# Kernel tuning notes

Hardware: AMD Instinct MI355X
Metric: run time of the kernel (lower is better)

Reference implementation:

```python
import jax, jax.numpy as jnp
import numpy as np

B, T, D = 64, 512, 1024

def setup_inputs() -> dict:
    key = jax.random.key(0)
    k1, k2, k3 = jax.random.split(key, 3)
    q1 = jax.random.normal(k1, (B, T, D), dtype=jnp.float32)
    q2 = jax.random.normal(k2, (B, T, D), dtype=jnp.float32)
    # original uses 'uniform' init; scale like a small uniform weight
    U = jax.random.uniform(k3, (D, D), dtype=jnp.float32, minval=-0.05, maxval=0.05)
    return {"q1": q1, "q2": q2, "U": U}

def reference(q1, q2, U):
    # bilinear scores: (q1 @ U) @ q2^T -> [B, T1, T2]
    att = jnp.einsum('btd,de,bse->bts', q1, U, q2)
    att = jax.nn.relu(att)
    w1_att = jax.nn.softmax(att, axis=1)  # softmax over q1 timesteps
    w2_att = jax.nn.softmax(att, axis=2)  # softmax over q2 timesteps
    # q1_align = w1_att^T @ q1 -> [B, T2, D]
    q1_align = jnp.einsum('bts,btd->bsd', w1_att, q1)
    # q2_align = w2_att @ q2 -> [B, T1, D]
    q2_align = jnp.einsum('bts,bsd->btd', w2_att, q2)
    return (q1_align, q2_align)
```

## Files before the change

kernel.cpp:

```cpp
#include <hip/hip_runtime.h>
#include <hip/hip_bf16.h>
#include <math.h>

#define B_DIM 64
#define T_DIM 512
#define D_DIM 1024
#define TT (T_DIM * T_DIM)
#define TD (T_DIM * D_DIM)
#define PSTR ((long)B_DIM * T_DIM)

typedef _Float16 f16;
typedef f16 f16x4 __attribute__((ext_vector_type(4)));
typedef f16 f16x8 __attribute__((ext_vector_type(8)));
typedef float f32x4 __attribute__((ext_vector_type(4)));

__device__ __forceinline__ void gld_lds16(const void* g, void* l) {
    __builtin_amdgcn_global_load_lds(
        (const __attribute__((address_space(1))) void*)g,
        (__attribute__((address_space(3))) void*)l, 16, 0, 0);
}

#define SWZ(r) (((r) >> 1) & 3)

__global__ __launch_bounds__(256) void k_d1(const float* __restrict__ q1,
                                            f16* __restrict__ q1ht,
                                            const float* __restrict__ U,
                                            f16* __restrict__ Uht) {
    __shared__ f16 tr[64][72];
    int tid = threadIdx.x;
    int z = blockIdx.z;
    if (z < 64) {
        int b = z;
        int d0 = blockIdx.x * 64, t0 = blockIdx.y * 64;
        const float* S = q1 + ((size_t)b * T_DIM + t0) * D_DIM + d0;
        int rr = tid >> 4, cc = (tid & 15) * 4;
#pragma unroll
        for (int i = 0; i < 4; ++i) {
            int r = rr + i * 16;
            float4 v = *(const float4*)(S + (size_t)r * D_DIM + cc);
            tr[cc + 0][r] = (f16)v.x;
            tr[cc + 1][r] = (f16)v.y;
            tr[cc + 2][r] = (f16)v.z;
            tr[cc + 3][r] = (f16)v.w;
        }
        __syncthreads();
        f16* Dt = q1ht + ((size_t)b * D_DIM + d0) * T_DIM + t0;
        int r2 = tid >> 3, c8 = (tid & 7) * 8;
#pragma unroll
        for (int i = 0; i < 2; ++i) {
            int d = r2 + i * 32;
            f16x8 vv = *(const f16x8*)(&tr[d][c8]);
            *(f16x8*)(Dt + (size_t)d * T_DIM + c8) = vv;
        }
    } else {
        int pos = blockIdx.y * 16 + blockIdx.x;
        for (int u = 0; u < 2; ++u) {
            int tile = pos + u * 128;
            int n0 = (tile & 15) * 64, k0 = (tile >> 4) * 64;
            int rr = tid >> 4, cc = (tid & 15) * 4;
#pragma unroll
            for (int i = 0; i < 4; ++i) {
                int r = rr + i * 16;
                float4 v = *(const float4*)(U + (size_t)(k0 + r) * D_DIM + n0 + cc);
                tr[cc + 0][r] = (f16)v.x;
                tr[cc + 1][r] = (f16)v.y;
                tr[cc + 2][r] = (f16)v.z;
                tr[cc + 3][r] = (f16)v.w;
            }
            __syncthreads();
            int r2 = tid >> 3, c8 = (tid & 7) * 8;
#pragma unroll
            for (int i = 0; i < 2; ++i) {
                int n = r2 + i * 32;
                f16x8 vv = *(const f16x8*)(&tr[n][c8]);
                *(f16x8*)(Uht + (size_t)(n0 + n) * D_DIM + k0 + c8) = vv;
            }
            __syncthreads();
        }
    }
}

__global__ __launch_bounds__(512, 2) void k_d2(const float* __restrict__ q1,
                                               const f16* __restrict__ Uht,
                                               f16* __restrict__ qUh,
                                               const float* __restrict__ q2,
                                               f16* __restrict__ q2h,
                                               f16* __restrict__ q2ht) {
    __shared__ __align__(16) f16 SM[32768];
    int tid = threadIdx.x;
    if (blockIdx.y < 128) {
        f16 (*LA)[8192] = (f16(*)[8192])SM;
        f16 (*LB)[8192] = (f16(*)[8192])(SM + 16384);
        const int lane = tid & 63, w = tid >> 6;
        int o = blockIdx.x + 4 * blockIdx.y;
        int fl = (o & 7) * 64 + (o >> 3);
        int bx = fl & 3, by = fl >> 2;
        const float* Aq = q1 + (long)(by * 256) * D_DIM;
        const f16* Bb = Uht + (long)(bx * 256) * D_DIM;

        const int r0 = tid >> 2, j0 = tid & 3;
        const int r1 = r0 + 128;
        const long srcA0 = (long)r0 * D_DIM + j0 * 8;
        const long srcA1 = (long)r1 * D_DIM + j0 * 8;
        const int wA0 = r0 * 32 + ((j0 ^ SWZ(r0)) << 3);
        const int wA1 = r1 * 32 + ((j0 ^ SWZ(r1)) << 3);
        const long offB0 = (long)r0 * D_DIM + (j0 ^ SWZ(r0)) * 8;
        const long offB1 = (long)r1 * D_DIM + (j0 ^ SWZ(r1)) * 8;
        const int ldsOff0 = w * 512, ldsOff1 = 4096 + w * 512;
        const int g = lane >> 4;
        const int rA0 = (w & 1) * 128 + (lane & 15);
        const int rB0 = (w >> 1) * 64 + (lane & 15);

        f32x4 acc[8][4] = {};
        {
            float4 v0 = *(const float4*)(Aq + srcA0);
            float4 v1 = *(const float4*)(Aq + srcA0 + 4);
            float4 v2 = *(const float4*)(Aq + srcA1);
            float4 v3 = *(const float4*)(Aq + srcA1 + 4);
            f16x8 h0 = {(f16)v0.x, (f16)v0.y, (f16)v0.z, (f16)v0.w,
                        (f16)v1.x, (f16)v1.y, (f16)v1.z, (f16)v1.w};
            f16x8 h1 = {(f16)v2.x, (f16)v2.y, (f16)v2.z, (f16)v2.w,
                        (f16)v3.x, (f16)v3.y, (f16)v3.z, (f16)v3.w};
            *(f16x8*)(&LA[0][wA0]) = h0;
            *(f16x8*)(&LA[0][wA1]) = h1;
            gld_lds16(Bb + offB0, &LB[0][ldsOff0]);
            gld_lds16(Bb + offB1, &LB[0][ldsOff1]);
        }
        __syncthreads();

        for (int t = 0; t < 32; ++t) {
            const int cur = t & 1;
            float4 v0, v1, v2, v3;
            if (t + 1 < 32) {
                const long kc = (long)(t + 1) << 5;
                v0 = *(const float4*)(Aq + srcA0 + kc);
                v1 = *(const float4*)(Aq + srcA0 + kc + 4);
                v2 = *(const float4*)(Aq + srcA1 + kc);
                v3 = *(const float4*)(Aq + srcA1 + kc + 4);
                gld_lds16(Bb + offB0 + kc, &LB[cur ^ 1][ldsOff0]);
                gld_lds16(Bb + offB1 + kc, &LB[cur ^ 1][ldsOff1]);
            }
            f16x8 a[8], b[4];
#pragma unroll
            for (int m = 0; m < 8; ++m) {
                int r = rA0 + m * 16;
                a[m] = *(const f16x8*)(&LA[cur][r * 32 + ((g ^ SWZ(r)) << 3)]);
            }
#pragma unroll
            for (int n = 0; n < 4; ++n) {
                int r = rB0 + n * 16;
                b[n] = *(const f16x8*)(&LB[cur][r * 32 + ((g ^ SWZ(r)) << 3)]);
            }
            __builtin_amdgcn_s_setprio(1);
#pragma unroll
            for (int m = 0; m < 8; ++m)
#pragma unroll
                for (int n = 0; n < 4; ++n)
                    acc[m][n] = __builtin_amdgcn_mfma_f32_16x16x32_f16(a[m], b[n], acc[m][n], 0, 0, 0);
            __builtin_amdgcn_s_setprio(0);
            if (t + 1 < 32) {
                f16x8 h0 = {(f16)v0.x, (f16)v0.y, (f16)v0.z, (f16)v0.w,
                            (f16)v1.x, (f16)v1.y, (f16)v1.z, (f16)v1.w};
                f16x8 h1 = {(f16)v2.x, (f16)v2.y, (f16)v2.z, (f16)v2.w,
                            (f16)v3.x, (f16)v3.y, (f16)v3.z, (f16)v3.w};
                *(f16x8*)(&LA[cur ^ 1][wA0]) = h0;
                *(f16x8*)(&LA[cur ^ 1][wA1]) = h1;
            }
            __syncthreads();
        }
        const int row0 = by * 256 + (w & 1) * 128 + (lane >> 4) * 4;
        const int col0 = bx * 256 + (w >> 1) * 64 + (lane & 15);
#pragma unroll
        for (int m = 0; m < 8; ++m)
#pragma unroll
            for (int r = 0; r < 4; ++r) {
                long row = row0 + m * 16 + r;
#pragma unroll
                for (int n = 0; n < 4; ++n)
                    qUh[row * D_DIM + col0 + n * 16] = (f16)acc[m][n][r];
            }
    } else {
        int hf = tid >> 8, t2 = tid & 255;
        f16 (*tr)[72] = (f16(*)[72])(SM + hf * 4608);
        int p = (blockIdx.y - 128) * 4 + blockIdx.x;
        int tile = p * 2 + hf;
        int b = tile >> 7, rem = tile & 127;
        int d0 = (rem & 15) * 64, t0 = (rem >> 4) * 64;
        const float* S = q2 + ((size_t)b * T_DIM + t0) * D_DIM + d0;
        f16* Dr = q2h + ((size_t)b * T_DIM + t0) * D_DIM + d0;
        int rr = t2 >> 4, cc = (t2 & 15) * 4;
#pragma unroll
        for (int i = 0; i < 4; ++i) {
            int r = rr + i * 16;
            float4 v = *(const float4*)(S + (size_t)r * D_DIM + cc);
            f16x4 h = {(f16)v.x, (f16)v.y, (f16)v.z, (f16)v.w};
            *(f16x4*)(Dr + (size_t)r * D_DIM + cc) = h;
            tr[cc + 0][r] = h[0];
            tr[cc + 1][r] = h[1];
            tr[cc + 2][r] = h[2];
            tr[cc + 3][r] = h[3];
        }
        __syncthreads();
        f16* Dt = q2ht + ((size_t)b * D_DIM + d0) * T_DIM + t0;
        int r2 = t2 >> 3, c8 = (t2 & 7) * 8;
#pragma unroll
        for (int i = 0; i < 2; ++i) {
            int d = r2 + i * 32;
            f16x8 vv = *(const f16x8*)(&tr[d][c8]);
            *(f16x8*)(Dt + (size_t)d * T_DIM + c8) = vv;
        }
    }
}

__global__ __launch_bounds__(512, 2) void k_att3(const f16* __restrict__ qUh,
                                                 const f16* __restrict__ q2h,
                                                 f16* __restrict__ P2,
                                                 f16* __restrict__ P1,
                                                 float2* __restrict__ rowP,
                                                 float2* __restrict__ colP) {
    __shared__ __align__(16) f16 LA[2][8192];
    __shared__ __align__(16) f16 LB[2][8192];
    const int tid = threadIdx.x;
    const int lane = tid & 63, w = tid >> 6;

    int o = blockIdx.x + 2 * (blockIdx.y + 2 * blockIdx.z);
    int fl = (o & 7) * 32 + (o >> 3);
    const int bx = fl & 1, by = (fl >> 1) & 1, zb = fl >> 2;

    const f16* Ab = qUh + (long)(zb * 512 + by * 256) * D_DIM;
    const f16* Bb = q2h + (long)zb * TD + (long)(bx * 256) * D_DIM;

    const int r0 = tid >> 2, j0 = tid & 3;
    const int r1 = r0 + 128;
    const long offA0 = (long)r0 * D_DIM + (j0 ^ SWZ(r0)) * 8;
    const long offA1 = (long)r1 * D_DIM + (j0 ^ SWZ(r1)) * 8;
    const int ldsOff0 = w * 512, ldsOff1 = 4096 + w * 512;
    const int g = lane >> 4;
    const int rA0 = (w & 1) * 128 + (lane & 15);
    const int rB0 = (w >> 1) * 64 + (lane & 15);

    f32x4 acc[8][4] = {};

    gld_lds16(Ab + offA0, &LA[0][ldsOff0]);
    gld_lds16(Ab + offA1, &LA[0][ldsOff1]);
    gld_lds16(Bb + offA0, &LB[0][ldsOff0]);
    gld_lds16(Bb + offA1, &LB[0][ldsOff1]);
    __syncthreads();

    for (int t = 0; t < 32; ++t) {
        const int cur = t & 1;
        if (t + 1 < 32) {
            const long kt = (long)(t + 1) << 5;
            gld_lds16(Ab + offA0 + kt, &LA[cur ^ 1][ldsOff0]);
            gld_lds16(Ab + offA1 + kt, &LA[cur ^ 1][ldsOff1]);
            gld_lds16(Bb + offA0 + kt, &LB[cur ^ 1][ldsOff0]);
            gld_lds16(Bb + offA1 + kt, &LB[cur ^ 1][ldsOff1]);
        }
        f16x8 a[8], b[4];
#pragma unroll
        for (int m = 0; m < 8; ++m) {
            int r = rA0 + m * 16;
            a[m] = *(const f16x8*)(&LA[cur][r * 32 + ((g ^ SWZ(r)) << 3)]);
        }
#pragma unroll
        for (int n = 0; n < 4; ++n) {
            int r = rB0 + n * 16;
            b[n] = *(const f16x8*)(&LB[cur][r * 32 + ((g ^ SWZ(r)) << 3)]);
        }
        __builtin_amdgcn_s_setprio(1);
#pragma unroll
        for (int m = 0; m < 8; ++m)
#pragma unroll
            for (int n = 0; n < 4; ++n)
                acc[m][n] = __builtin_amdgcn_mfma_f32_16x16x32_f16(a[m], b[n], acc[m][n], 0, 0, 0);
        __builtin_amdgcn_s_setprio(0);
        __syncthreads();
    }

#pragma unroll
    for (int m = 0; m < 8; ++m)
#pragma unroll
        for (int n = 0; n < 4; ++n)
#pragma unroll
            for (int r = 0; r < 4; ++r)
                acc[m][n][r] = fmaxf(acc[m][n][r], 0.0f);

    float* redR = (float*)(&LA[0][0]);
    float* redC = redR + 2048;
    float* rowM = redC + 1024;
    float* colM = rowM + 256;
    const int h = w & 1, cw = w >> 1;
#pragma unroll
    for (int m = 0; m < 8; ++m)
#pragma unroll
        for (int r = 0; r < 4; ++r) {
            float mx = fmaxf(fmaxf(acc[m][0][r], acc[m][1][r]),
                             fmaxf(acc[m][2][r], acc[m][3][r]));
            mx = fmaxf(mx, __shfl_xor(mx, 1));
            mx = fmaxf(mx, __shfl_xor(mx, 2));
            mx = fmaxf(mx, __shfl_xor(mx, 4));
            mx = fmaxf(mx, __shfl_xor(mx, 8));
            float sm = __expf(acc[m][0][r] - mx) + __expf(acc[m][1][r] - mx)
                     + __expf(acc[m][2][r] - mx) + __expf(acc[m][3][r] - mx);
            sm += __shfl_xor(sm, 1);
            sm += __shfl_xor(sm, 2);
            sm += __shfl_xor(sm, 4);
            sm += __shfl_xor(sm, 8);
            if ((lane & 15) == 0) {
                int lr = m * 16 + (lane >> 4) * 4 + r;
                redR[((h * 128 + lr) * 4 + cw) * 2 + 0] = mx;
                redR[((h * 128 + lr) * 4 + cw) * 2 + 1] = sm;
            }
        }
#pragma unroll
    for (int n = 0; n < 4; ++n) {
        float mx = acc[0][n][0];
#pragma unroll
        for (int m = 0; m < 8; ++m)
#pragma unroll
            for (int r = 0; r < 4; ++r) mx = fmaxf(mx, acc[m][n][r]);
        mx = fmaxf(mx, __shfl_xor(mx, 16));
        mx = fmaxf(mx, __shfl_xor(mx, 32));
        float sm = 0.f;
#pragma unroll
        for (int m = 0; m < 8; ++m)
#pragma unroll
            for (int r = 0; r < 4; ++r) sm += __expf(acc[m][n][r] - mx);
        sm += __shfl_xor(sm, 16);
        sm += __shfl_xor(sm, 32);
        if (lane < 16) {
            int c = cw * 64 + n * 16 + lane;
            redC[(h * 256 + c) * 2 + 0] = mx;
            redC[(h * 256 + c) * 2 + 1] = sm;
        }
    }
    __syncthreads();
    if (tid < 256) {
        float M = -1e30f, S = 0.f;
#pragma unroll
        for (int i = 0; i < 4; ++i) {
            float m_ = redR[(tid * 4 + i) * 2 + 0];
            float s_ = redR[(tid * 4 + i) * 2 + 1];
            float nm = fmaxf(M, m_);
            S = S * __expf(M - nm) + s_ * __expf(m_ - nm);
            M = nm;
        }
        rowP[(long)bx * PSTR + (long)zb * 512 + by * 256 + tid] = make_float2(M, S);
        rowM[tid] = M;
    } else {
        int c = tid - 256;
        float m0_ = redC[c * 2 + 0], s0_ = redC[c * 2 + 1];
        float m1_ = redC[(256 + c) * 2 + 0], s1_ = redC[(256 + c) * 2 + 1];
        float M = fmaxf(m0_, m1_);
        float S = s0_ * __expf(m0_ - M) + s1_ * __expf(m1_ - M);
        colP[(long)by * PSTR + (long)zb * 512 + bx * 256 + c] = make_float2(M, S);
        colM[c] = M;
    }
    __syncthreads();

    f16* P2b = P2 + (long)zb * TT;
#pragma unroll
    for (int m = 0; m < 8; ++m)
#pragma unroll
        for (int r = 0; r < 4; ++r) {
            int Lr = h * 128 + m * 16 + (lane >> 4) * 4 + r;
            float M = rowM[Lr];
            long base = (long)(by * 256 + Lr) * T_DIM + bx * 256;
#pragma unroll
            for (int n = 0; n < 4; ++n) {
                int c = cw * 64 + n * 16 + (lane & 15);
                P2b[base + c] = (f16)__expf(acc[m][n][r] - M);
            }
        }
    f16* P1b = P1 + (long)zb * TT;
#pragma unroll
    for (int m = 0; m < 8; ++m) {
        int Lt = h * 128 + m * 16 + (lane >> 4) * 4;
#pragma unroll
        for (int n = 0; n < 4; ++n) {
            int Lc = cw * 64 + n * 16 + (lane & 15);
            float M = colM[Lc];
            f16x4 v = {(f16)__expf(acc[m][n][0] - M), (f16)__expf(acc[m][n][1] - M),
                       (f16)__expf(acc[m][n][2] - M), (f16)__expf(acc[m][n][3] - M)};
            *(f16x4*)(&P1b[(long)(bx * 256 + Lc) * T_DIM + by * 256 + Lt]) = v;
        }
    }
}

__global__ __launch_bounds__(512, 2) void k_align(
        const f16* __restrict__ P2, const f16* __restrict__ q2ht,
        const float2* __restrict__ rowP, float* __restrict__ outQ2,
        const f16* __restrict__ P1, const f16* __restrict__ q1ht,
        const float2* __restrict__ colP, float* __restrict__ outQ1) {
    __shared__ __align__(16) f16 LA[2][8192];
    __shared__ __align__(16) f16 LB[2][8192];
    const int tid = threadIdx.x;
    const int lane = tid & 63, w = tid >> 6;

    int o = blockIdx.x + 4 * (blockIdx.y + 2 * blockIdx.z);
    int fl = (o & 7) * 128 + (o >> 3);
    const int bx = fl & 3, by = (fl >> 2) & 1, z = fl >> 3;
    const int zb = z & 63;

    const f16* P  = (z < 64) ? P2 : P1;
    const f16* Bt = (z < 64) ? q2ht : q1ht;
    const float2* sp = ((z < 64) ? rowP : colP) + (long)zb * 512;
    float* out = ((z < 64) ? outQ2 : outQ1) + (long)zb * TD;

    const f16* Ab = P + (long)zb * TT + (long)(by * 256) * T_DIM;
    const f16* Bb = Bt + (long)zb * TD + (long)(bx * 256) * T_DIM;

    const int r0 = tid >> 2, j0 = tid & 3;
    const int r1 = r0 + 128;
    float2 pa0 = sp[by * 256 + r0], pb0 = sp[PSTR + by * 256 + r0];
    float M0 = fmaxf(pa0.x, pb0.x);
    f16 f00 = (f16)__expf(pa0.x - M0), f01 = (f16)__expf(pb0.x - M0);
    float2 pa1 = sp[by * 256 + r1], pb1 = sp[PSTR + by * 256 + r1];
    float M1 = fmaxf(pa1.x, pb1.x);
    f16 f10 = (f16)__expf(pa1.x - M1), f11 = (f16)__expf(pb1.x - M1);

    const long srcA0 = (long)r0 * T_DIM + j0 * 8;
    const long srcA1 = (long)r1 * T_DIM + j0 * 8;
    const int wA0 = r0 * 32 + ((j0 ^ SWZ(r0)) << 3);
    const int wA1 = r1 * 32 + ((j0 ^ SWZ(r1)) << 3);
    const long offB0 = (long)r0 * T_DIM + (j0 ^ SWZ(r0)) * 8;
    const long offB1 = (long)r1 * T_DIM + (j0 ^ SWZ(r1)) * 8;
    const int ldsOff0 = w * 512, ldsOff1 = 4096 + w * 512;
    const int g = lane >> 4;
    const int rA0 = (w & 1) * 128 + (lane & 15);
    const int rB0 = (w >> 1) * 64 + (lane & 15);

    f32x4 acc[8][4] = {};
    {
        f16x8 a0 = *(const f16x8*)(Ab + srcA0);
        f16x8 a1 = *(const f16x8*)(Ab + srcA1);
#pragma unroll
        for (int i = 0; i < 8; ++i) { a0[i] *= f00; a1[i] *= f10; }
        *(f16x8*)(&LA[0][wA0]) = a0;
        *(f16x8*)(&LA[0][wA1]) = a1;
        gld_lds16(Bb + offB0, &LB[0][ldsOff0]);
        gld_lds16(Bb + offB1, &LB[0][ldsOff1]);
    }
    __syncthreads();

    for (int t = 0; t < 16; ++t) {
        const int cur = t & 1;
        f16x8 a0n, a1n;
        if (t + 1 < 16) {
            const long kc = (long)(t + 1) << 5;
            a0n = *(const f16x8*)(Ab + srcA0 + kc);
            a1n = *(const f16x8*)(Ab + srcA1 + kc);
            gld_lds16(Bb + offB0 + kc, &LB[cur ^ 1][ldsOff0]);
            gld_lds16(Bb + offB1 + kc, &LB[cur ^ 1][ldsOff1]);
        }
        f16x8 a[8], b[4];
#pragma unroll
        for (int m = 0; m < 8; ++m) {
            int r = rA0 + m * 16;
            a[m] = *(const f16x8*)(&LA[cur][r * 32 + ((g ^ SWZ(r)) << 3)]);
        }
#pragma unroll
        for (int n = 0; n < 4; ++n) {
            int r = rB0 + n * 16;
            b[n] = *(const f16x8*)(&LB[cur][r * 32 + ((g ^ SWZ(r)) << 3)]);
        }
        __builtin_amdgcn_s_setprio(1);
#pragma unroll
        for (int m = 0; m < 8; ++m)
#pragma unroll
            for (int n = 0; n < 4; ++n)
                acc[m][n] = __builtin_amdgcn_mfma_f32_16x16x32_f16(a[m], b[n], acc[m][n], 0, 0, 0);
        __builtin_amdgcn_s_setprio(0);
        if (t + 1 < 16) {
            f16 fa = ((t + 1) & 8) ? f01 : f00;
            f16 fb = ((t + 1) & 8) ? f11 : f10;
#pragma unroll
            for (int i = 0; i < 8; ++i) { a0n[i] *= fa; a1n[i] *= fb; }
            *(f16x8*)(&LA[cur ^ 1][wA0]) = a0n;
            *(f16x8*)(&LA[cur ^ 1][wA1]) = a1n;
        }
        __syncthreads();
    }

    const int row0 = by * 256 + (w & 1) * 128 + (lane >> 4) * 4;
    const int col0 = bx * 256 + (w >> 1) * 64 + (lane & 15);
#pragma unroll
    for (int m = 0; m < 8; ++m)
#pragma unroll
        for (int r = 0; r < 4; ++r) {
            int row = row0 + m * 16 + r;
            float2 pa = sp[row], pb = sp[PSTR + row];
            float M = fmaxf(pa.x, pb.x);
            float S = pa.y * __expf(pa.x - M) + pb.y * __expf(pb.x - M);
            float inv = 1.0f / S;
#pragma unroll
            for (int n = 0; n < 4; ++n)
                out[(long)row * D_DIM + col0 + n * 16] = acc[m][n][r] * inv;
        }
}

extern "C" void kernel_launch(void* const* d_in, const int* in_sizes, int n_in,
                              void* d_out, int out_size, void* d_ws, size_t ws_size,
                              hipStream_t stream) {
    const float* q1 = (const float*)d_in[0];
    const float* q2 = (const float*)d_in[1];
    const float* U  = (const float*)d_in[2];
    float* out = (float*)d_out;

    const size_t BTD = (size_t)B_DIM * TD;
    const size_t DD  = (size_t)D_DIM * D_DIM;
    const size_t BTT = (size_t)B_DIM * TT;

    const size_t need = (4 * BTD + DD) * 2
                      + 2 * BTT * 2
                      + 4 * (size_t)PSTR * sizeof(float2);
    if (need > ws_size) return;

    f16* q1ht = (f16*)d_ws;
    f16* q2h  = q1ht + BTD;
    f16* q2ht = q2h  + BTD;
    f16* Uht  = q2ht + BTD;
    f16* qUh  = Uht  + DD;
    f16* P2   = qUh  + BTD;
    f16* P1   = P2   + BTT;
    float2* rowP = (float2*)(P1 + BTT);
    float2* colP = rowP + 2 * (size_t)PSTR;

    k_d1<<<dim3(16, 8, 65), 256, 0, stream>>>(q1, q1ht, U, Uht);
    k_d2<<<dim3(4, 128 + 1024, 1), 512, 0, stream>>>(q1, Uht, qUh, q2, q2h, q2ht);
    k_att3<<<dim3(2, 2, 64), 512, 0, stream>>>(qUh, q2h, P2, P1, rowP, colP);
    k_align<<<dim3(4, 2, 128), 512, 0, stream>>>(
        P2, q2ht, rowP, out + BTD, P1, q1ht, colP, out);
}
```

Measured before the change: 387.6 us.

## Drop q2 fp16 copy; cast q2 inside attention GEMM and move transpose into cast kernel

The row-major fp16 copy of q2 (q2h) is no longer materialized. The attention-score kernel now reads q2 as fp32 from global memory and converts it to fp16 in registers before the swizzled LDS store, the same way the first GEMM already handles q1. The q2 transpose-cast moves into the first cast kernel alongside q1, so the qU GEMM kernel no longer shares a launch with the cast blocks. This removes a BTD-sized fp16 write and read, but k_att3 now reads fp32 (twice the bytes) for its B operand and does register conversions instead of direct global-to-LDS loads.

```diff
diff --git a/kernel.cpp b/kernel.cpp
--- a/kernel.cpp
+++ b/kernel.cpp
@@ -22,17 +22,21 @@
 
 #define SWZ(r) (((r) >> 1) & 3)
 
-__global__ __launch_bounds__(256) void k_d1(const float* __restrict__ q1,
-                                            f16* __restrict__ q1ht,
-                                            const float* __restrict__ U,
-                                            f16* __restrict__ Uht) {
+__global__ __launch_bounds__(256) void k_cast(const float* __restrict__ q1,
+                                              f16* __restrict__ q1ht,
+                                              const float* __restrict__ q2,
+                                              f16* __restrict__ q2ht,
+                                              const float* __restrict__ U,
+                                              f16* __restrict__ Uht) {
     __shared__ f16 tr[64][72];
     int tid = threadIdx.x;
     int z = blockIdx.z;
-    if (z < 64) {
-        int b = z;
+    if (z < 128) {
+        const float* src = (z < 64) ? q1 : q2;
+        f16* dstT = (z < 64) ? q1ht : q2ht;
+        int b = z & 63;
         int d0 = blockIdx.x * 64, t0 = blockIdx.y * 64;
-        const float* S = q1 + ((size_t)b * T_DIM + t0) * D_DIM + d0;
+        const float* S = src + ((size_t)b * T_DIM + t0) * D_DIM + d0;
         int rr = tid >> 4, cc = (tid & 15) * 4;
 #pragma unroll
         for (int i = 0; i < 4; ++i) {
@@ -44,7 +48,7 @@
             tr[cc + 3][r] = (f16)v.w;
         }
         __syncthreads();
-        f16* Dt = q1ht + ((size_t)b * D_DIM + d0) * T_DIM + t0;
+        f16* Dt = dstT + ((size_t)b * D_DIM + d0) * T_DIM + t0;
         int r2 = tid >> 3, c8 = (tid & 7) * 8;
 #pragma unroll
         for (int i = 0; i < 2; ++i) {
@@ -80,140 +84,104 @@
     }
 }
 
-__global__ __launch_bounds__(512, 2) void k_d2(const float* __restrict__ q1,
-                                               const f16* __restrict__ Uht,
-                                               f16* __restrict__ qUh,
-                                               const float* __restrict__ q2,
-                                               f16* __restrict__ q2h,
-                                               f16* __restrict__ q2ht) {
-    __shared__ __align__(16) f16 SM[32768];
-    int tid = threadIdx.x;
-    if (blockIdx.y < 128) {
-        f16 (*LA)[8192] = (f16(*)[8192])SM;
-        f16 (*LB)[8192] = (f16(*)[8192])(SM + 16384);
-        const int lane = tid & 63, w = tid >> 6;
-        int o = blockIdx.x + 4 * blockIdx.y;
-        int fl = (o & 7) * 64 + (o >> 3);
-        int bx = fl & 3, by = fl >> 2;
-        const float* Aq = q1 + (long)(by * 256) * D_DIM;
-        const f16* Bb = Uht + (long)(bx * 256) * D_DIM;
-
-        const int r0 = tid >> 2, j0 = tid & 3;
-        const int r1 = r0 + 128;
-        const long srcA0 = (long)r0 * D_DIM + j0 * 8;
-        const long srcA1 = (long)r1 * D_DIM + j0 * 8;
-        const int wA0 = r0 * 32 + ((j0 ^ SWZ(r0)) << 3);
-        const int wA1 = r1 * 32 + ((j0 ^ SWZ(r1)) << 3);
-        const long offB0 = (long)r0 * D_DIM + (j0 ^ SWZ(r0)) * 8;
-        const long offB1 = (long)r1 * D_DIM + (j0 ^ SWZ(r1)) * 8;
-        const int ldsOff0 = w * 512, ldsOff1 = 4096 + w * 512;
-        const int g = lane >> 4;
-        const int rA0 = (w & 1) * 128 + (lane & 15);
-        const int rB0 = (w >> 1) * 64 + (lane & 15);
-
-        f32x4 acc[8][4] = {};
-        {
-            float4 v0 = *(const float4*)(Aq + srcA0);
-            float4 v1 = *(const float4*)(Aq + srcA0 + 4);
-            float4 v2 = *(const float4*)(Aq + srcA1);
-            float4 v3 = *(const float4*)(Aq + srcA1 + 4);
+__global__ __launch_bounds__(512, 2) void k_gemm1(const float* __restrict__ q1,
+                                                  const f16* __restrict__ Uht,
+                                                  f16* __restrict__ qUh) {
+    __shared__ __align__(16) f16 LA[2][8192];
+    __shared__ __align__(16) f16 LB[2][8192];
+    const int tid = threadIdx.x;
+    const int lane = tid & 63, w = tid >> 6;
+    int o = blockIdx.x + 4 * blockIdx.y;
+    int fl = (o & 7) * 64 + (o >> 3);
+    int bx = fl & 3, by = fl >> 2;
+    const float* Aq = q1 + (long)(by * 256) * D_DIM;
+    const f16* Bb = Uht + (long)(bx * 256) * D_DIM;
+
+    const int r0 = tid >> 2, j0 = tid & 3;
+    const int r1 = r0 + 128;
+    const long srcA0 = (long)r0 * D_DIM + j0 * 8;
+    const long srcA1 = (long)r1 * D_DIM + j0 * 8;
+    const int wA0 = r0 * 32 + ((j0 ^ SWZ(r0)) << 3);
+    const int wA1 = r1 * 32 + ((j0 ^ SWZ(r1)) << 3);
+    const long offB0 = (long)r0 * D_DIM + (j0 ^ SWZ(r0)) * 8;
+    const long offB1 = (long)r1 * D_DIM + (j0 ^ SWZ(r1)) * 8;
+    const int ldsOff0 = w * 512, ldsOff1 = 4096 + w * 512;
+    const int g = lane >> 4;
+    const int rA0 = (w & 1) * 128 + (lane & 15);
+    const int rB0 = (w >> 1) * 64 + (lane & 15);
+
+    f32x4 acc[8][4] = {};
+    {
+        float4 v0 = *(const float4*)(Aq + srcA0);
+        float4 v1 = *(const float4*)(Aq + srcA0 + 4);
+        float4 v2 = *(const float4*)(Aq + srcA1);
+        float4 v3 = *(const float4*)(Aq + srcA1 + 4);
+        f16x8 h0 = {(f16)v0.x, (f16)v0.y, (f16)v0.z, (f16)v0.w,
+                    (f16)v1.x, (f16)v1.y, (f16)v1.z, (f16)v1.w};
+        f16x8 h1 = {(f16)v2.x, (f16)v2.y, (f16)v2.z, (f16)v2.w,
+                    (f16)v3.x, (f16)v3.y, (f16)v3.z, (f16)v3.w};
+        *(f16x8*)(&LA[0][wA0]) = h0;
+        *(f16x8*)(&LA[0][wA1]) = h1;
+        gld_lds16(Bb + offB0, &LB[0][ldsOff0]);
+        gld_lds16(Bb + offB1, &LB[0][ldsOff1]);
+    }
+    __syncthreads();
+
+    for (int t = 0; t < 32; ++t) {
+        const int cur = t & 1;
+        float4 v0, v1, v2, v3;
+        if (t + 1 < 32) {
+            const long kc = (long)(t + 1) << 5;
+            v0 = *(const float4*)(Aq + srcA0 + kc);
+            v1 = *(const float4*)(Aq + srcA0 + kc + 4);
+            v2 = *(const float4*)(Aq + srcA1 + kc);
+            v3 = *(const float4*)(Aq + srcA1 + kc + 4);
+            gld_lds16(Bb + offB0 + kc, &LB[cur ^ 1][ldsOff0]);
+            gld_lds16(Bb + offB1 + kc, &LB[cur ^ 1][ldsOff1]);
+        }
+        f16x8 a[8], b[4];
+#pragma unroll
+        for (int m = 0; m < 8; ++m) {
+            int r = rA0 + m * 16;
+            a[m] = *(const f16x8*)(&LA[cur][r * 32 + ((g ^ SWZ(r)) << 3)]);
+        }
+#pragma unroll
+        for (int n = 0; n < 4; ++n) {
+            int r = rB0 + n * 16;
+            b[n] = *(const f16x8*)(&LB[cur][r * 32 + ((g ^ SWZ(r)) << 3)]);
+        }
+        __builtin_amdgcn_s_setprio(1);
+#pragma unroll
+        for (int m = 0; m < 8; ++m)
+#pragma unroll
+            for (int n = 0; n < 4; ++n)
+                acc[m][n] = __builtin_amdgcn_mfma_f32_16x16x32_f16(a[m], b[n], acc[m][n], 0, 0, 0);
+        __builtin_amdgcn_s_setprio(0);
+        if (t + 1 < 32) {
             f16x8 h0 = {(f16)v0.x, (f16)v0.y, (f16)v0.z, (f16)v0.w,
                         (f16)v1.x, (f16)v1.y, (f16)v1.z, (f16)v1.w};
             f16x8 h1 = {(f16)v2.x, (f16)v2.y, (f16)v2.z, (f16)v2.w,
                         (f16)v3.x, (f16)v3.y, (f16)v3.z, (f16)v3.w};
-            *(f16x8*)(&LA[0][wA0]) = h0;
-            *(f16x8*)(&LA[0][wA1]) = h1;
-            gld_lds16(Bb + offB0, &LB[0][ldsOff0]);
-            gld_lds16(Bb + offB1, &LB[0][ldsOff1]);
+            *(f16x8*)(&LA[cur ^ 1][wA0]) = h0;
+            *(f16x8*)(&LA[cur ^ 1][wA1]) = h1;
         }
         __syncthreads();
-
-        for (int t = 0; t < 32; ++t) {
-            const int cur = t & 1;
-            float4 v0, v1, v2, v3;
-            if (t + 1 < 32) {
-                const long kc = (long)(t + 1) << 5;
-                v0 = *(const float4*)(Aq + srcA0 + kc);
-                v1 = *(const float4*)(Aq + srcA0 + kc + 4);
-                v2 = *(const float4*)(Aq + srcA1 + kc);
-                v3 = *(const float4*)(Aq + srcA1 + kc + 4);
-                gld_lds16(Bb + offB0 + kc, &LB[cur ^ 1][ldsOff0]);
-                gld_lds16(Bb + offB1 + kc, &LB[cur ^ 1][ldsOff1]);
-            }
-            f16x8 a[8], b[4];
-#pragma unroll
-            for (int m = 0; m < 8; ++m) {
-                int r = rA0 + m * 16;
-                a[m] = *(const f16x8*)(&LA[cur][r * 32 + ((g ^ SWZ(r)) << 3)]);
-            }
-#pragma unroll
-            for (int n = 0; n < 4; ++n) {
-                int r = rB0 + n * 16;
-                b[n] = *(const f16x8*)(&LB[cur][r * 32 + ((g ^ SWZ(r)) << 3)]);
-            }
-            __builtin_amdgcn_s_setprio(1);
-#pragma unroll
-            for (int m = 0; m < 8; ++m)
-#pragma unroll
-                for (int n = 0; n < 4; ++n)
-                    acc[m][n] = __builtin_amdgcn_mfma_f32_16x16x32_f16(a[m], b[n], acc[m][n], 0, 0, 0);
-            __builtin_amdgcn_s_setprio(0);
-            if (t + 1 < 32) {
-                f16x8 h0 = {(f16)v0.x, (f16)v0.y, (f16)v0.z, (f16)v0.w,
-                            (f16)v1.x, (f16)v1.y, (f16)v1.z, (f16)v1.w};
-                f16x8 h1 = {(f16)v2.x, (f16)v2.y, (f16)v2.z, (f16)v2.w,
-                            (f16)v3.x, (f16)v3.y, (f16)v3.z, (f16)v3.w};
-                *(f16x8*)(&LA[cur ^ 1][wA0]) = h0;
-                *(f16x8*)(&LA[cur ^ 1][wA1]) = h1;
-            }
-            __syncthreads();
-        }
-        const int row0 = by * 256 + (w & 1) * 128 + (lane >> 4) * 4;
-        const int col0 = bx * 256 + (w >> 1) * 64 + (lane & 15);
-#pragma unroll
-        for (int m = 0; m < 8; ++m)
-#pragma unroll
-            for (int r = 0; r < 4; ++r) {
-                long row = row0 + m * 16 + r;
-#pragma unroll
-                for (int n = 0; n < 4; ++n)
-                    qUh[row * D_DIM + col0 + n * 16] = (f16)acc[m][n][r];
-            }
-    } else {
-        int hf = tid >> 8, t2 = tid & 255;
-        f16 (*tr)[72] = (f16(*)[72])(SM + hf * 4608);
-        int p = (blockIdx.y - 128) * 4 + blockIdx.x;
-        int tile = p * 2 + hf;
-        int b = tile >> 7, rem = tile & 127;
-        int d0 = (rem & 15) * 64, t0 = (rem >> 4) * 64;
-        const float* S = q2 + ((size_t)b * T_DIM + t0) * D_DIM + d0;
-        f16* Dr = q2h + ((size_t)b * T_DIM + t0) * D_DIM + d0;
-        int rr = t2 >> 4, cc = (t2 & 15) * 4;
-#pragma unroll
-        for (int i = 0; i < 4; ++i) {
-            int r = rr + i * 16;
-            float4 v = *(const float4*)(S + (size_t)r * D_DIM + cc);
-            f16x4 h = {(f16)v.x, (f16)v.y, (f16)v.z, (f16)v.w};
-            *(f16x4*)(Dr + (size_t)r * D_DIM + cc) = h;
-            tr[cc + 0][r] = h[0];
-            tr[cc + 1][r] = h[1];
-            tr[cc + 2][r] = h[2];
-            tr[cc + 3][r] = h[3];
-        }
-        __syncthreads();
-        f16* Dt = q2ht + ((size_t)b * D_DIM + d0) * T_DIM + t0;
-        int r2 = t2 >> 3, c8 = (t2 & 7) * 8;
-#pragma unroll
-        for (int i = 0; i < 2; ++i) {
-            int d = r2 + i * 32;
-            f16x8 vv = *(const f16x8*)(&tr[d][c8]);
-            *(f16x8*)(Dt + (size_t)d * T_DIM + c8) = vv;
-        }
-    }
+    }
+    const int row0 = by * 256 + (w & 1) * 128 + (lane >> 4) * 4;
+    const int col0 = bx * 256 + (w >> 1) * 64 + (lane & 15);
+#pragma unroll
+    for (int m = 0; m < 8; ++m)
+#pragma unroll
+        for (int r = 0; r < 4; ++r) {
+            long row = row0 + m * 16 + r;
+#pragma unroll
+            for (int n = 0; n < 4; ++n)
+                qUh[row * D_DIM + col0 + n * 16] = (f16)acc[m][n][r];
+        }
 }
 
 __global__ __launch_bounds__(512, 2) void k_att3(const f16* __restrict__ qUh,
-                                                 const f16* __restrict__ q2h,
+                                                 const float* __restrict__ q2,
                                                  f16* __restrict__ P2,
                                                  f16* __restrict__ P1,
                                                  float2* __restrict__ rowP,
@@ -228,12 +196,16 @@
     const int bx = fl & 1, by = (fl >> 1) & 1, zb = fl >> 2;
 
     const f16* Ab = qUh + (long)(zb * 512 + by * 256) * D_DIM;
-    const f16* Bb = q2h + (long)zb * TD + (long)(bx * 256) * D_DIM;
+    const float* Bq = q2 + (long)zb * TD + (long)(bx * 256) * D_DIM;
 
     const int r0 = tid >> 2, j0 = tid & 3;
     const int r1 = r0 + 128;
     const long offA0 = (long)r0 * D_DIM + (j0 ^ SWZ(r0)) * 8;
     const long offA1 = (long)r1 * D_DIM + (j0 ^ SWZ(r1)) * 8;
+    const long srcB0 = (long)r0 * D_DIM + j0 * 8;
+    const long srcB1 = (long)r1 * D_DIM + j0 * 8;
+    const int wB0 = r0 * 32 + ((j0 ^ SWZ(r0)) << 3);
+    const int wB1 = r1 * 32 + ((j0 ^ SWZ(r1)) << 3);
     const int ldsOff0 = w * 512, ldsOff1 = 4096 + w * 512;
     const int g = lane >> 4;
     const int rA0 = (w & 1) * 128 + (lane & 15);
@@ -241,20 +213,33 @@
 
     f32x4 acc[8][4] = {};
 
-    gld_lds16(Ab + offA0, &LA[0][ldsOff0]);
-    gld_lds16(Ab + offA1, &LA[0][ldsOff1]);
-    gld_lds16(Bb + offA0, &LB[0][ldsOff0]);
-    gld_lds16(Bb + offA1, &LB[0][ldsOff1]);
+    {
+        gld_lds16(Ab + offA0, &LA[0][ldsOff0]);
+        gld_lds16(Ab + offA1, &LA[0][ldsOff1]);
+        float4 v0 = *(const float4*)(Bq + srcB0);
+        float4 v1 = *(const float4*)(Bq + srcB0 + 4);
+        float4 v2 = *(const float4*)(Bq + srcB1);
+        float4 v3 = *(const float4*)(Bq + srcB1 + 4);
+        f16x8 h0 = {(f16)v0.x, (f16)v0.y, (f16)v0.z, (f16)v0.w,
+                    (f16)v1.x, (f16)v1.y, (f16)v1.z, (f16)v1.w};
+        f16x8 h1 = {(f16)v2.x, (f16)v2.y, (f16)v2.z, (f16)v2.w,
+                    (f16)v3.x, (f16)v3.y, (f16)v3.z, (f16)v3.w};
+        *(f16x8*)(&LB[0][wB0]) = h0;
+        *(f16x8*)(&LB[0][wB1]) = h1;
+    }
     __syncthreads();
 
     for (int t = 0; t < 32; ++t) {
         const int cur = t & 1;
+        float4 v0, v1, v2, v3;
         if (t + 1 < 32) {
             const long kt = (long)(t + 1) << 5;
             gld_lds16(Ab + offA0 + kt, &LA[cur ^ 1][ldsOff0]);
             gld_lds16(Ab + offA1 + kt, &LA[cur ^ 1][ldsOff1]);
-            gld_lds16(Bb + offA0 + kt, &LB[cur ^ 1][ldsOff0]);
-            gld_lds16(Bb + offA1 + kt, &LB[cur ^ 1][ldsOff1]);
+            v0 = *(const float4*)(Bq + srcB0 + kt);
+            v1 = *(const float4*)(Bq + srcB0 + kt + 4);
+            v2 = *(const float4*)(Bq + srcB1 + kt);
+            v3 = *(const float4*)(Bq + srcB1 + kt + 4);
         }
         f16x8 a[8], b[4];
 #pragma unroll
@@ -274,6 +259,14 @@
             for (int n = 0; n < 4; ++n)
                 acc[m][n] = __builtin_amdgcn_mfma_f32_16x16x32_f16(a[m], b[n], acc[m][n], 0, 0, 0);
         __builtin_amdgcn_s_setprio(0);
+        if (t + 1 < 32) {
+            f16x8 h0 = {(f16)v0.x, (f16)v0.y, (f16)v0.z, (f16)v0.w,
+                        (f16)v1.x, (f16)v1.y, (f16)v1.z, (f16)v1.w};
+            f16x8 h1 = {(f16)v2.x, (f16)v2.y, (f16)v2.z, (f16)v2.w,
+                        (f16)v3.x, (f16)v3.y, (f16)v3.z, (f16)v3.w};
+            *(f16x8*)(&LB[cur ^ 1][wB0]) = h0;
+            *(f16x8*)(&LB[cur ^ 1][wB1]) = h1;
+        }
         __syncthreads();
     }
 
@@ -511,14 +504,13 @@
     const size_t DD  = (size_t)D_DIM * D_DIM;
     const size_t BTT = (size_t)B_DIM * TT;
 
-    const size_t need = (4 * BTD + DD) * 2
+    const size_t need = (3 * BTD + DD) * 2
                       + 2 * BTT * 2
                       + 4 * (size_t)PSTR * sizeof(float2);
     if (need > ws_size) return;
 
     f16* q1ht = (f16*)d_ws;
-    f16* q2h  = q1ht + BTD;
-    f16* q2ht = q2h  + BTD;
+    f16* q2ht = q1ht + BTD;
     f16* Uht  = q2ht + BTD;
     f16* qUh  = Uht  + DD;
     f16* P2   = qUh  + BTD;
@@ -526,9 +518,9 @@
     float2* rowP = (float2*)(P1 + BTT);
     float2* colP = rowP + 2 * (size_t)PSTR;
 
-    k_d1<<<dim3(16, 8, 65), 256, 0, stream>>>(q1, q1ht, U, Uht);
-    k_d2<<<dim3(4, 128 + 1024, 1), 512, 0, stream>>>(q1, Uht, qUh, q2, q2h, q2ht);
-    k_att3<<<dim3(2, 2, 64), 512, 0, stream>>>(qUh, q2h, P2, P1, rowP, colP);
+    k_cast<<<dim3(16, 8, 129), 256, 0, stream>>>(q1, q1ht, q2, q2ht, U, Uht);
+    k_gemm1<<<dim3(4, 128), 512, 0, stream>>>(q1, Uht, qUh);
+    k_att3<<<dim3(2, 2, 64), 512, 0, stream>>>(qUh, q2, P2, P1, rowP, colP);
     k_align<<<dim3(4, 2, 128), 512, 0, stream>>>(
         P2, q2ht, rowP, out + BTD, P1, q1ht, colP, out);
 }
```

Result: slower. 442.0 us (+14.0%).
